# Performance work log

Hardware: AMD Instinct MI355X
Metric: run time of the kernel (lower is better)

## Reference

```python
import jax, jax.numpy as jnp
import numpy as np

LOG2PI = 1.8378770664093453


def setup_inputs() -> dict:
    key = jax.random.key(0)
    ks = jax.random.split(key, 8)
    B, IN, OUT = 16384, 2048, 1
    x = jax.random.normal(ks[0], (B, IN), dtype=jnp.float32)
    y = jax.random.normal(ks[1], (B, OUT), dtype=jnp.float32)
    counter = jax.random.uniform(ks[2], (B,), dtype=jnp.float32)
    # learned params (flax init: zeros / normal(stddev=0.01) / normal/in_features)
    noise_mean = jnp.zeros((OUT,), dtype=jnp.float32)
    noise_logdiag = 0.01 * jax.random.normal(ks[3], (OUT,), dtype=jnp.float32)
    W_mean = 0.01 * jax.random.normal(ks[4], (OUT, IN), dtype=jnp.float32)
    W_logdiag = 0.01 * jax.random.normal(ks[5], (OUT, IN), dtype=jnp.float32)
    W_offdiag = jax.random.normal(ks[6], (OUT, IN, IN), dtype=jnp.float32) / IN
    return {"x": x, "y": y, "counter": counter,
            "noise_mean": noise_mean, "noise_logdiag": noise_logdiag,
            "W_mean": W_mean, "W_logdiag": W_logdiag, "W_offdiag": W_offdiag}


def reference(x, y, counter, noise_mean, noise_logdiag, W_mean, W_logdiag, W_offdiag):
    # hyperparams matching init_kwargs
    regularization_weight = 0.0001
    prior_scale = 1.0
    wishart_scale = 0.01
    dof = 1.0
    in_f = x.shape[-1]
    out_f = W_mean.shape[0]
    adjusted_dof = (dof + out_f + 1.0) / 2.0

    # Cholesky factor of W covariance: strict lower triangle + exp(logdiag) on diag
    L = jnp.tril(W_offdiag, k=-1) + jnp.exp(W_logdiag)[..., None] * jnp.eye(in_f, dtype=x.dtype)  # (out,in,in)

    # predictive mean under W_mean; diagonal noise
    pred_mean = x @ W_mean.T  # (B,out)
    pred_likelihood = (-0.5 * ((y - pred_mean) / jnp.exp(noise_logdiag)) ** 2
                       - noise_logdiag - 0.5 * LOG2PI)  # (B,out) elementwise Gaussian logpdf

    # covariance-weighted inner product: (L^T b)^2 summed, b = counter-scaled x
    x_mod = x * counter[:, None]  # (B,in)
    Ltb = jnp.einsum('oij,bi->boj', L, x_mod)  # (B,out,in)
    quad = jnp.sum(Ltb * Ltb, axis=-1)  # (B,out) = b^T L L^T b per out
    noise_prec = jnp.exp(-2.0 * noise_logdiag)  # (out,)
    trace_term = 0.5 * quad * noise_prec  # (B,out)

    # KL(q(W) || N(0, prior_scale I))
    mse_term = jnp.sum(W_mean ** 2) / prior_scale
    trace_cov = jnp.sum(L * L, axis=(-1, -2))  # (out,)
    logdet_cov = 2.0 * jnp.sum(W_logdiag, axis=-1)  # (out,)
    kl_term = 0.5 * (mse_term + jnp.sum(trace_cov) / prior_scale
                     + jnp.sum(in_f * jnp.log(prior_scale) - logdet_cov))

    # Wishart prior terms on noise precision
    logdet_precision = jnp.sum(-2.0 * noise_logdiag)
    trace_precision = jnp.sum(noise_prec)
    wishart_term = adjusted_dof * logdet_precision - 0.5 * wishart_scale * trace_precision

    total_elbo = jnp.sum((pred_likelihood.squeeze() - trace_term.squeeze()) * counter) / jnp.sum(counter)
    total_elbo = total_elbo + regularization_weight * (wishart_term - kl_term)
    return -total_elbo
```

## Files before the change

### kernel.cpp

```cpp
#include <hip/hip_runtime.h>
#include <hip/hip_bf16.h>
#include <math.h>

#define LOG2PI_F 1.8378770664093453f

typedef int i32x4 __attribute__((ext_vector_type(4)));
typedef int i32x8 __attribute__((ext_vector_type(8)));
typedef float f32x4 __attribute__((ext_vector_type(4)));

#define M_DIM 16384
#define K_DIM 2048
#define N_DIM 2048
#define BM 256
#define BN 256
#define BK 128
#define NB_N (N_DIM / BN)
#define NB_M (M_DIM / BM)
#define LSCALE 256.0f
#define QDESCALE (1.0f / 65536.0f)
#define SCALE_ONE 0x7F7F7F7F

__device__ __forceinline__ void gload16(const void* g, void* l) {
    __builtin_amdgcn_global_load_lds(
        (__attribute__((address_space(1))) void*)g,
        (__attribute__((address_space(3))) void*)l, 16, 0, 0);
}

__device__ __forceinline__ unsigned int pk4_fp8(float a, float b, float c, float d) {
    unsigned int w = (unsigned int)__builtin_amdgcn_cvt_pk_fp8_f32(a, b, 0, false);
    w = (unsigned int)__builtin_amdgcn_cvt_pk_fp8_f32(c, d, (int)w, true);
    return w;
}

__global__ __launch_bounds__(256) void prep_fused(const float* __restrict__ X,
                                                  const float* __restrict__ Wm,
                                                  const float* __restrict__ Woff,
                                                  const float* __restrict__ Wld,
                                                  unsigned char* __restrict__ Xq,
                                                  unsigned char* __restrict__ Lq,
                                                  float* __restrict__ U,
                                                  float* __restrict__ misc_arr) {
    __shared__ float tile[64][65];
    __shared__ float red[4];
    const int bid = blockIdx.x;
    const int tid = threadIdx.x;

    if (bid < 1024) {
        const int jt = (bid & 31) * 64;
        const int it = (bid >> 5) * 64;
        float ss = 0.f;

        if (it + 63 >= jt) {
            for (int e = tid; e < 4096; e += 256) {
                int r = e >> 6, c = e & 63;
                tile[r][c] = Woff[(size_t)(it + r) * K_DIM + (jt + c)];
            }
        }
        __syncthreads();

        for (int e = tid; e < 4096; e += 256) {
            int jr = e >> 6, ic = e & 63;
            int i = it + ic, j = jt + jr;
            float v = 0.f;
            if (i > j) {
                v = tile[ic][jr];
                ss += v * v;
            } else if (i == j) {
                v = expf(Wld[i]);
            }
            unsigned int w = (unsigned int)__builtin_amdgcn_cvt_pk_fp8_f32(v * LSCALE, 0.f, 0, false);
            Lq[(size_t)j * K_DIM + i] = (unsigned char)(w & 0xffu);
        }

        #pragma unroll
        for (int off = 32; off; off >>= 1) ss += __shfl_down(ss, off);
        if ((tid & 63) == 0) red[tid >> 6] = ss;
        __syncthreads();
        if (tid == 0)
            misc_arr[bid] = red[0] + red[1] + red[2] + red[3];
    } else {
        const int b = bid - 1024;
        const float* xr = X + (size_t)b * K_DIM;
        unsigned char* xo = Xq + (size_t)b * K_DIM;
        const int base = tid * 8;
        float4 v0 = *(const float4*)(xr + base);
        float4 v1 = *(const float4*)(xr + base + 4);
        float4 w0 = *(const float4*)(Wm + base);
        float4 w1 = *(const float4*)(Wm + base + 4);
        float dot = v0.x * w0.x + v0.y * w0.y + v0.z * w0.z + v0.w * w0.w
                  + v1.x * w1.x + v1.y * w1.y + v1.z * w1.z + v1.w * w1.w;
        uint2 p;
        p.x = pk4_fp8(v0.x, v0.y, v0.z, v0.w);
        p.y = pk4_fp8(v1.x, v1.y, v1.z, v1.w);
        *(uint2*)(xo + base) = p;
        #pragma unroll
        for (int off = 32; off; off >>= 1) dot += __shfl_down(dot, off);
        if ((tid & 63) == 0) red[tid >> 6] = dot;
        __syncthreads();
        if (tid == 0) U[b] = red[0] + red[1] + red[2] + red[3];
    }
}

__device__ __forceinline__ i32x8 frag128(const unsigned char* base, int roff, int g) {
    const unsigned char* rb = base + roff * 128;
    int x = (roff & 7) << 4;
    i32x4 lo = *(const i32x4*)(rb + (((g * 2) << 4) ^ x));
    i32x4 hi = *(const i32x4*)(rb + (((g * 2 + 1) << 4) ^ x));
    return __builtin_shufflevector(lo, hi, 0, 1, 2, 3, 4, 5, 6, 7);
}

#define MXMFMA(A, B, C) __builtin_amdgcn_mfma_scale_f32_16x16x128_f8f6f4( \
        (A), (B), (C), 0, 0, 0, SCALE_ONE, 0, SCALE_ONE)

#define BAR() asm volatile("s_barrier" ::: "memory")
#define WAITL() { asm volatile("s_waitcnt lgkmcnt(0)" ::: "memory"); \
                  __builtin_amdgcn_sched_barrier(0); }

__global__ __launch_bounds__(512, 2) void quad_gemm(const unsigned char* __restrict__ Xq,
                                                    const unsigned char* __restrict__ Lq,
                                                    float* __restrict__ qpart) {
    __shared__ unsigned char As[2][BM * BK];
    __shared__ unsigned char Bs[2][BN * BK];

    const int mb = blockIdx.x;
    const int jp = blockIdx.y;
    const int tid = threadIdx.x;
    const int lane = tid & 63;
    const int wid = tid >> 6;
    const int wr = wid >> 2, wc = wid & 3;
    const int g = lane >> 4, r16 = lane & 15;
    const int brow = mb * BM;

    const int srow = lane >> 3;
    const int scol = (lane & 7) ^ srow;

    auto gemm_one = [&](int nb) {
        const int bcol = nb * BN;
        const int NT = (K_DIM - bcol) >> 7;

        const unsigned char* pA[2];
        const unsigned char* pB[2];
        #pragma unroll
        for (int h = 0; h < 2; ++h) {
            pA[h] = Xq + (size_t)(brow + h * 128 + wid * 16 + srow) * K_DIM + bcol + scol * 16;
            pB[h] = Lq + (size_t)(bcol + h * 128 + wid * 16 + srow) * K_DIM + bcol + scol * 16;
        }

        auto stgA = [&](int t, int h, int buf) {
            const unsigned char* s = pA[h] + (size_t)t * 128;
            char* d = (char*)As[buf] + h * 16384 + wid * 2048;
            gload16(s, d);
            gload16(s + (size_t)8 * K_DIM, d + 1024);
        };
        auto stgB = [&](int t, int h, int buf) {
            const unsigned char* s = pB[h] + (size_t)t * 128;
            char* d = (char*)Bs[buf] + h * 16384 + wid * 2048;
            gload16(s, d);
            gload16(s + (size_t)8 * K_DIM, d + 1024);
        };

        f32x4 acc[8][4];
        const f32x4 zero = {0.f, 0.f, 0.f, 0.f};
        #pragma unroll
        for (int m = 0; m < 8; ++m)
            #pragma unroll
            for (int n = 0; n < 4; ++n) acc[m][n] = zero;

        stgA(0, 0, 0); stgA(0, 1, 0); stgB(0, 0, 0); stgB(0, 1, 0);
        stgB(1, 0, 1); stgB(1, 1, 1);
        asm volatile("s_waitcnt vmcnt(4)" ::: "memory");
        BAR();

        for (int t = 0; t < NT; ++t) {
            const int cur = t & 1, nbuf = cur ^ 1;
            const unsigned char* Abase = As[cur] + wr * 16384;
            const unsigned char* Bbase = Bs[cur] + (wc >> 1) * 16384;
            const int brow2 = (wc & 1) * 64;
            const bool s1 = (t + 1 < NT), s2 = (t + 2 < NT);
            i32x8 bf[4], af[4];

            #pragma unroll
            for (int n = 0; n < 4; ++n) bf[n] = frag128(Bbase, brow2 + n * 16 + r16, g);
            #pragma unroll
            for (int m = 0; m < 4; ++m) af[m] = frag128(Abase, m * 16 + r16, g);
            if (s1) { stgA(t + 1, 0, nbuf); stgA(t + 1, 1, nbuf); }
            BAR();
            WAITL();
            __builtin_amdgcn_s_setprio(1);
            #pragma unroll
            for (int m = 0; m < 4; ++m)
                #pragma unroll
                for (int n = 0; n < 4; ++n)
                    acc[m][n] = MXMFMA(af[m], bf[n], acc[m][n]);
            __builtin_amdgcn_s_setprio(0);
            BAR();

            #pragma unroll
            for (int m = 0; m < 4; ++m) af[m] = frag128(Abase, 64 + m * 16 + r16, g);
            if (s2) { stgB(t + 2, 0, cur); stgB(t + 2, 1, cur); }
            BAR();
            WAITL();
            __builtin_amdgcn_s_setprio(1);
            #pragma unroll
            for (int m = 0; m < 4; ++m)
                #pragma unroll
                for (int n = 0; n < 4; ++n)
                    acc[4 + m][n] = MXMFMA(af[m], bf[n], acc[4 + m][n]);
            __builtin_amdgcn_s_setprio(0);

            if (s2)
                asm volatile("s_waitcnt vmcnt(4)" ::: "memory");
            else if (s1)
                asm volatile("s_waitcnt vmcnt(0)" ::: "memory");
            BAR();
        }

        float* qbuf = (float*)&As[0][0];
        __syncthreads();
        #pragma unroll
        for (int m = 0; m < 8; ++m) {
            #pragma unroll
            for (int r = 0; r < 4; ++r) {
                float s = 0.f;
                #pragma unroll
                for (int n = 0; n < 4; ++n) {
                    float t = acc[m][n][r];
                    s += t * t;
                }
                #pragma unroll
                for (int off = 1; off < 16; off <<= 1) s += __shfl_xor(s, off);
                if (r16 == 0) qbuf[wc * 256 + wr * 128 + m * 16 + g * 4 + r] = s;
            }
        }
        __syncthreads();
        if (tid < BM)
            qpart[(size_t)(brow + tid) * NB_N + nb] =
                (qbuf[tid] + qbuf[256 + tid] + qbuf[512 + tid] + qbuf[768 + tid]) * QDESCALE;
        __syncthreads();
    };

    gemm_one(jp);
    gemm_one(7 - jp);
}
#undef BAR
#undef WAITL

__global__ __launch_bounds__(256) void row_part(const float* __restrict__ Y,
                                                const float* __restrict__ Cnt,
                                                const float* __restrict__ nld_p,
                                                const float* __restrict__ U,
                                                const float* __restrict__ qpart,
                                                double* __restrict__ dpart) {
    const int tid = threadIdx.x;
    const float nld = nld_p[0];
    const float inv_sig = expf(-nld);
    const float nprec = inv_sig * inv_sig;
    double s1 = 0.0, s2 = 0.0;
    const int base = blockIdx.x * 512;
    #pragma unroll
    for (int j = 0; j < 2; ++j) {
        int b = base + j * 256 + tid;
        float c = Cnt[b];
        const float4* qp = (const float4*)(qpart + (size_t)b * NB_N);
        float4 q0 = qp[0], q1 = qp[1];
        float q = q0.x + q0.y + q0.z + q0.w + q1.x + q1.y + q1.z + q1.w;
        float d = (Y[b] - U[b]) * inv_sig;
        float pl = -0.5f * d * d - nld - 0.5f * LOG2PI_F;
        float tt = 0.5f * q * c * c * nprec;
        s1 += (double)c;
        s2 += (double)((pl - tt) * c);
    }
    __shared__ double red[2][4];
    #pragma unroll
    for (int off = 32; off; off >>= 1) {
        s1 += __shfl_down(s1, off);
        s2 += __shfl_down(s2, off);
    }
    if ((tid & 63) == 0) { red[0][tid >> 6] = s1; red[1][tid >> 6] = s2; }
    __syncthreads();
    if (tid == 0) {
        dpart[blockIdx.x * 2 + 0] = red[0][0] + red[0][1] + red[0][2] + red[0][3];
        dpart[blockIdx.x * 2 + 1] = red[1][0] + red[1][1] + red[1][2] + red[1][3];
    }
}

__global__ __launch_bounds__(256) void finalize2(const float* __restrict__ nld_p,
                                                 const float* __restrict__ Wm,
                                                 const float* __restrict__ Wld,
                                                 const double* __restrict__ dpart,
                                                 const float* __restrict__ misc_arr,
                                                 float* __restrict__ out) {
    const int tid = threadIdx.x;
    const float nld = nld_p[0];
    const float inv_sig = expf(-nld);
    const float nprec = inv_sig * inv_sig;

    double s1 = 0.0, s2 = 0.0;
    if (tid < 32) { s1 = dpart[tid * 2]; s2 = dpart[tid * 2 + 1]; }

    double wm2 = 0.0, tcd = 0.0, wls = 0.0, offs = 0.0;
    for (int i = tid; i < K_DIM; i += 256) {
        float w = Wm[i];
        wm2 += (double)w * (double)w;
        float ld = Wld[i];
        tcd += exp(2.0 * (double)ld);
        wls += (double)ld;
    }
    for (int i = tid; i < 1024; i += 256) offs += (double)misc_arr[i];

    __shared__ double red[6][4];
    double vals[6] = {s1, s2, wm2, tcd, wls, offs};
    #pragma unroll
    for (int s = 0; s < 6; ++s) {
        double v = vals[s];
        #pragma unroll
        for (int off = 32; off; off >>= 1) v += __shfl_down(v, off);
        if ((tid & 63) == 0) red[s][tid >> 6] = v;
    }
    __syncthreads();
    if (tid == 0) {
        double S1 = red[0][0] + red[0][1] + red[0][2] + red[0][3];
        double S2 = red[1][0] + red[1][1] + red[1][2] + red[1][3];
        double MSE = red[2][0] + red[2][1] + red[2][2] + red[2][3];
        double TCD = red[3][0] + red[3][1] + red[3][2] + red[3][3];
        double WLS = red[4][0] + red[4][1] + red[4][2] + red[4][3];
        double OFFS = red[5][0] + red[5][1] + red[5][2] + red[5][3];

        double trace_cov = OFFS + TCD;
        double kl = 0.5 * (MSE + trace_cov - 2.0 * WLS);
        double wish = 1.5 * (-2.0 * (double)nld) - 0.005 * (double)nprec;
        double elbo = S2 / S1 + 1e-4 * (wish - kl);
        out[0] = (float)(-elbo);
    }
}

extern "C" void kernel_launch(void* const* d_in, const int* in_sizes, int n_in,
                              void* d_out, int out_size, void* d_ws, size_t ws_size,
                              hipStream_t stream) {
    const float* x    = (const float*)d_in[0];
    const float* y    = (const float*)d_in[1];
    const float* cnt  = (const float*)d_in[2];
    const float* nld  = (const float*)d_in[4];
    const float* Wm   = (const float*)d_in[5];
    const float* Wld  = (const float*)d_in[6];
    const float* Woff = (const float*)d_in[7];

    char* ws = (char*)d_ws;
    unsigned char* Xq = (unsigned char*)(ws);
    unsigned char* Lq = (unsigned char*)(ws + 33554432);
    double* dpart  = (double*)(ws + 40000000);
    float*  U      = (float*)(ws + 75497472);
    float*  qpart  = (float*)(ws + 75563008);
    float*  misc   = (float*)(ws + 76611584);

    prep_fused<<<dim3(1024 + M_DIM), 256, 0, stream>>>(x, Wm, Woff, Wld, Xq, Lq, U, misc);
    quad_gemm<<<dim3(NB_M, 4), 512, 0, stream>>>(Xq, Lq, qpart);
    row_part<<<dim3(32), 256, 0, stream>>>(y, cnt, nld, U, qpart, dpart);
    finalize2<<<1, 256, 0, stream>>>(nld, Wm, Wld, dpart, misc, (float*)d_out);
}
```

Baseline: 87.69 us.

## Fuse row reduction and finalize into GEMM via last-block atomic counters

Merges the row_part and finalize2 kernels into the tail of the quad GEMM kernel. A per-row-block atomic counter lets the last of the four column blocks reduce its rows, and a global counter lets the last row block compute the final scalar. This removes two kernel launches and their gaps but adds a memset, thread fences and atomics to the GEMM kernel.

```diff
diff --git a/kernel.cpp b/kernel.cpp
--- a/kernel.cpp
+++ b/kernel.cpp
@@ -49,7 +49,6 @@
         const int jt = (bid & 31) * 64;
         const int it = (bid >> 5) * 64;
         float ss = 0.f;
-
         if (it + 63 >= jt) {
             for (int e = tid; e < 4096; e += 256) {
                 int r = e >> 6, c = e & 63;
@@ -57,27 +56,20 @@
             }
         }
         __syncthreads();
-
         for (int e = tid; e < 4096; e += 256) {
             int jr = e >> 6, ic = e & 63;
             int i = it + ic, j = jt + jr;
             float v = 0.f;
-            if (i > j) {
-                v = tile[ic][jr];
-                ss += v * v;
-            } else if (i == j) {
-                v = expf(Wld[i]);
-            }
+            if (i > j) { v = tile[ic][jr]; ss += v * v; }
+            else if (i == j) v = expf(Wld[i]);
             unsigned int w = (unsigned int)__builtin_amdgcn_cvt_pk_fp8_f32(v * LSCALE, 0.f, 0, false);
             Lq[(size_t)j * K_DIM + i] = (unsigned char)(w & 0xffu);
         }
-
         #pragma unroll
         for (int off = 32; off; off >>= 1) ss += __shfl_down(ss, off);
         if ((tid & 63) == 0) red[tid >> 6] = ss;
         __syncthreads();
-        if (tid == 0)
-            misc_arr[bid] = red[0] + red[1] + red[2] + red[3];
+        if (tid == 0) misc_arr[bid] = red[0] + red[1] + red[2] + red[3];
     } else {
         const int b = bid - 1024;
         const float* xr = X + (size_t)b * K_DIM;
@@ -111,16 +103,27 @@
 
 #define MXMFMA(A, B, C) __builtin_amdgcn_mfma_scale_f32_16x16x128_f8f6f4( \
         (A), (B), (C), 0, 0, 0, SCALE_ONE, 0, SCALE_ONE)
-
 #define BAR() asm volatile("s_barrier" ::: "memory")
 #define WAITL() { asm volatile("s_waitcnt lgkmcnt(0)" ::: "memory"); \
                   __builtin_amdgcn_sched_barrier(0); }
 
-__global__ __launch_bounds__(512, 2) void quad_gemm(const unsigned char* __restrict__ Xq,
-                                                    const unsigned char* __restrict__ Lq,
-                                                    float* __restrict__ qpart) {
+__global__ __launch_bounds__(512, 2) void quad_all(const unsigned char* __restrict__ Xq,
+                                                   const unsigned char* __restrict__ Lq,
+                                                   float* __restrict__ qpart,
+                                                   const float* __restrict__ Y,
+                                                   const float* __restrict__ Cnt,
+                                                   const float* __restrict__ nld_p,
+                                                   const float* __restrict__ U,
+                                                   const float* __restrict__ Wm,
+                                                   const float* __restrict__ Wld,
+                                                   const float* __restrict__ misc,
+                                                   double* __restrict__ dpart,
+                                                   int* __restrict__ mbcnt,
+                                                   int* __restrict__ gcnt,
+                                                   float* __restrict__ out) {
     __shared__ unsigned char As[2][BM * BK];
     __shared__ unsigned char Bs[2][BN * BK];
+    __shared__ int s_f1, s_f2;
 
     const int mb = blockIdx.x;
     const int jp = blockIdx.y;
@@ -130,7 +133,6 @@
     const int wr = wid >> 2, wc = wid & 3;
     const int g = lane >> 4, r16 = lane & 15;
     const int brow = mb * BM;
-
     const int srow = lane >> 3;
     const int scol = (lane & 7) ^ srow;
 
@@ -145,7 +147,6 @@
             pA[h] = Xq + (size_t)(brow + h * 128 + wid * 16 + srow) * K_DIM + bcol + scol * 16;
             pB[h] = Lq + (size_t)(bcol + h * 128 + wid * 16 + srow) * K_DIM + bcol + scol * 16;
         }
-
         auto stgA = [&](int t, int h, int buf) {
             const unsigned char* s = pA[h] + (size_t)t * 128;
             char* d = (char*)As[buf] + h * 16384 + wid * 2048;
@@ -208,10 +209,8 @@
                     acc[4 + m][n] = MXMFMA(af[m], bf[n], acc[4 + m][n]);
             __builtin_amdgcn_s_setprio(0);
 
-            if (s2)
-                asm volatile("s_waitcnt vmcnt(4)" ::: "memory");
-            else if (s1)
-                asm volatile("s_waitcnt vmcnt(0)" ::: "memory");
+            if (s2)      asm volatile("s_waitcnt vmcnt(4)" ::: "memory");
+            else if (s1) asm volatile("s_waitcnt vmcnt(0)" ::: "memory");
             BAR();
         }
 
@@ -224,8 +223,8 @@
                 float s = 0.f;
                 #pragma unroll
                 for (int n = 0; n < 4; ++n) {
-                    float t = acc[m][n][r];
-                    s += t * t;
+                    float t2 = acc[m][n][r];
+                    s += t2 * t2;
                 }
                 #pragma unroll
                 for (int off = 1; off < 16; off <<= 1) s += __shfl_xor(s, off);
@@ -241,98 +240,99 @@
 
     gemm_one(jp);
     gemm_one(7 - jp);
-}
-#undef BAR
-#undef WAITL
-
-__global__ __launch_bounds__(256) void row_part(const float* __restrict__ Y,
-                                                const float* __restrict__ Cnt,
-                                                const float* __restrict__ nld_p,
-                                                const float* __restrict__ U,
-                                                const float* __restrict__ qpart,
-                                                double* __restrict__ dpart) {
-    const int tid = threadIdx.x;
+
+    __threadfence();
+    if (tid == 0)
+        s_f1 = __hip_atomic_fetch_add(&mbcnt[mb], 1, __ATOMIC_ACQ_REL, __HIP_MEMORY_SCOPE_AGENT);
+    __syncthreads();
+    if (s_f1 != 3) return;
+
     const float nld = nld_p[0];
     const float inv_sig = expf(-nld);
     const float nprec = inv_sig * inv_sig;
+
     double s1 = 0.0, s2 = 0.0;
-    const int base = blockIdx.x * 512;
-    #pragma unroll
-    for (int j = 0; j < 2; ++j) {
-        int b = base + j * 256 + tid;
-        float c = Cnt[b];
-        const float4* qp = (const float4*)(qpart + (size_t)b * NB_N);
+    if (tid < 256) {
+        const int row = brow + tid;
+        const float4* qp = (const float4*)(qpart + (size_t)row * NB_N);
         float4 q0 = qp[0], q1 = qp[1];
         float q = q0.x + q0.y + q0.z + q0.w + q1.x + q1.y + q1.z + q1.w;
-        float d = (Y[b] - U[b]) * inv_sig;
+        float c = Cnt[row];
+        float d = (Y[row] - U[row]) * inv_sig;
         float pl = -0.5f * d * d - nld - 0.5f * LOG2PI_F;
         float tt = 0.5f * q * c * c * nprec;
-        s1 += (double)c;
-        s2 += (double)((pl - tt) * c);
-    }
-    __shared__ double red[2][4];
+        s1 = (double)c;
+        s2 = (double)((pl - tt) * c);
+    }
     #pragma unroll
     for (int off = 32; off; off >>= 1) {
         s1 += __shfl_down(s1, off);
         s2 += __shfl_down(s2, off);
     }
-    if ((tid & 63) == 0) { red[0][tid >> 6] = s1; red[1][tid >> 6] = s2; }
+    {
+        double* dred = (double*)&As[0][0];
+        if (lane == 0) { dred[wid] = s1; dred[8 + wid] = s2; }
+        __syncthreads();
+        if (tid == 0) {
+            double S1 = 0.0, S2 = 0.0;
+            #pragma unroll
+            for (int w2 = 0; w2 < 8; ++w2) { S1 += dred[w2]; S2 += dred[8 + w2]; }
+            dpart[mb * 2 + 0] = S1;
+            dpart[mb * 2 + 1] = S2;
+        }
+    }
     __syncthreads();
-    if (tid == 0) {
-        dpart[blockIdx.x * 2 + 0] = red[0][0] + red[0][1] + red[0][2] + red[0][3];
-        dpart[blockIdx.x * 2 + 1] = red[1][0] + red[1][1] + red[1][2] + red[1][3];
-    }
-}
-
-__global__ __launch_bounds__(256) void finalize2(const float* __restrict__ nld_p,
-                                                 const float* __restrict__ Wm,
-                                                 const float* __restrict__ Wld,
-                                                 const double* __restrict__ dpart,
-                                                 const float* __restrict__ misc_arr,
-                                                 float* __restrict__ out) {
-    const int tid = threadIdx.x;
-    const float nld = nld_p[0];
-    const float inv_sig = expf(-nld);
-    const float nprec = inv_sig * inv_sig;
-
-    double s1 = 0.0, s2 = 0.0;
-    if (tid < 32) { s1 = dpart[tid * 2]; s2 = dpart[tid * 2 + 1]; }
+
+    __threadfence();
+    if (tid == 0)
+        s_f2 = __hip_atomic_fetch_add(gcnt, 1, __ATOMIC_ACQ_REL, __HIP_MEMORY_SCOPE_AGENT);
+    __syncthreads();
+    if (s_f2 != NB_M - 1) return;
+
+    double f1 = 0.0, f2 = 0.0;
+    if (tid < NB_M) { f1 = dpart[tid * 2]; f2 = dpart[tid * 2 + 1]; }
 
     double wm2 = 0.0, tcd = 0.0, wls = 0.0, offs = 0.0;
-    for (int i = tid; i < K_DIM; i += 256) {
+    for (int i = tid; i < K_DIM; i += 512) {
         float w = Wm[i];
         wm2 += (double)w * (double)w;
         float ld = Wld[i];
         tcd += exp(2.0 * (double)ld);
         wls += (double)ld;
     }
-    for (int i = tid; i < 1024; i += 256) offs += (double)misc_arr[i];
-
-    __shared__ double red[6][4];
-    double vals[6] = {s1, s2, wm2, tcd, wls, offs};
-    #pragma unroll
-    for (int s = 0; s < 6; ++s) {
-        double v = vals[s];
-        #pragma unroll
-        for (int off = 32; off; off >>= 1) v += __shfl_down(v, off);
-        if ((tid & 63) == 0) red[s][tid >> 6] = v;
-    }
-    __syncthreads();
-    if (tid == 0) {
-        double S1 = red[0][0] + red[0][1] + red[0][2] + red[0][3];
-        double S2 = red[1][0] + red[1][1] + red[1][2] + red[1][3];
-        double MSE = red[2][0] + red[2][1] + red[2][2] + red[2][3];
-        double TCD = red[3][0] + red[3][1] + red[3][2] + red[3][3];
-        double WLS = red[4][0] + red[4][1] + red[4][2] + red[4][3];
-        double OFFS = red[5][0] + red[5][1] + red[5][2] + red[5][3];
-
-        double trace_cov = OFFS + TCD;
-        double kl = 0.5 * (MSE + trace_cov - 2.0 * WLS);
-        double wish = 1.5 * (-2.0 * (double)nld) - 0.005 * (double)nprec;
-        double elbo = S2 / S1 + 1e-4 * (wish - kl);
-        out[0] = (float)(-elbo);
-    }
-}
+    for (int i = tid; i < 1024; i += 512) offs += (double)misc[i];
+
+    {
+        double* dred = (double*)&As[0][0];
+        double vals[6] = {f1, f2, wm2, tcd, wls, offs};
+        __syncthreads();
+        #pragma unroll
+        for (int s = 0; s < 6; ++s) {
+            double v = vals[s];
+            #pragma unroll
+            for (int off = 32; off; off >>= 1) v += __shfl_down(v, off);
+            if (lane == 0) dred[s * 8 + wid] = v;
+        }
+        __syncthreads();
+        if (tid == 0) {
+            double a6[6];
+            #pragma unroll
+            for (int s = 0; s < 6; ++s) {
+                double v = 0.0;
+                #pragma unroll
+                for (int w2 = 0; w2 < 8; ++w2) v += dred[s * 8 + w2];
+                a6[s] = v;
+            }
+            double trace_cov = a6[5] + a6[3];
+            double kl = 0.5 * (a6[2] + trace_cov - 2.0 * a6[4]);
+            double wish = 1.5 * (-2.0 * (double)nld) - 0.005 * (double)nprec;
+            double elbo = a6[1] / a6[0] + 1e-4 * (wish - kl);
+            out[0] = (float)(-elbo);
+        }
+    }
+}
+#undef BAR
+#undef WAITL
 
 extern "C" void kernel_launch(void* const* d_in, const int* in_sizes, int n_in,
                               void* d_out, int out_size, void* d_ws, size_t ws_size,
@@ -349,12 +349,16 @@
     unsigned char* Xq = (unsigned char*)(ws);
     unsigned char* Lq = (unsigned char*)(ws + 33554432);
     double* dpart  = (double*)(ws + 40000000);
+    int*    mbcnt  = (int*)(ws + 40008192);
+    int*    gcnt   = (int*)(ws + 40008448);
     float*  U      = (float*)(ws + 75497472);
     float*  qpart  = (float*)(ws + 75563008);
     float*  misc   = (float*)(ws + 76611584);
+    float*  outp   = (float*)d_out;
+
+    hipMemsetAsync(ws + 40008192, 0, 512, stream);
 
     prep_fused<<<dim3(1024 + M_DIM), 256, 0, stream>>>(x, Wm, Woff, Wld, Xq, Lq, U, misc);
-    quad_gemm<<<dim3(NB_M, 4), 512, 0, stream>>>(Xq, Lq, qpart);
-    row_part<<<dim3(32), 256, 0, stream>>>(y, cnt, nld, U, qpart, dpart);
-    finalize2<<<1, 256, 0, stream>>>(nld, Wm, Wld, dpart, misc, (float*)d_out);
-}
+    quad_all<<<dim3(NB_M, 4), 512, 0, stream>>>(Xq, Lq, qpart, y, cnt, nld, U,
+                                                Wm, Wld, misc, dpart, mbcnt, gcnt, outp);
+}
```

After: 132.1 us. +50.7%, slower.
